# Kernel optimization log

Hardware: AMD Instinct MI355X
Metric: run time of the kernel (lower is better)

The kernel has to match this reference:

```python
import jax, jax.numpy as jnp
import numpy as np

B, S, D, H = 2, 2048, 1024, 16
HD = D // H  # 64
SCALE = HD ** -0.5


def setup_inputs() -> dict:
    key = jax.random.key(0)
    ks = jax.random.split(key, 11)
    std = D ** -0.5
    inp = {
        "q": jax.random.normal(ks[0], (B, S, D), jnp.float32),
        "k": jax.random.normal(ks[1], (B, S, D), jnp.float32),
        "v": jax.random.normal(ks[2], (B, S, D), jnp.float32),
        # causal mask: True = masked (strictly upper triangular)
        "attn_mask": jnp.triu(jnp.ones((S, S), jnp.bool_), k=1),
        "Wq": jax.random.normal(ks[3], (D, D), jnp.float32) * std,
        "bq": jnp.zeros((D,), jnp.float32),
        "Wk": jax.random.normal(ks[4], (D, D), jnp.float32) * std,
        "bk": jnp.zeros((D,), jnp.float32),
        "Wv": jax.random.normal(ks[5], (D, D), jnp.float32) * std,
        "bv": jnp.zeros((D,), jnp.float32),
        "Wo": jax.random.normal(ks[6], (D, D), jnp.float32) * std,
        "bo": jnp.zeros((D,), jnp.float32),
    }
    return inp


def reference(q, k, v, attn_mask, Wq, bq, Wk, bk, Wv, bv, Wo, bo):
    # projections (torch Linear: x @ W.T + b), split into heads: [B,H,S,HD]
    def heads(x, W, b):
        y = jnp.einsum("bsd,ed->bse", x, W) + b
        return y.reshape(B, S, H, HD).transpose(0, 2, 1, 3)

    qh = heads(q, Wq, bq)
    kh = heads(k, Wk, bk)
    vh = heads(v, Wv, bv)

    # scaled dot-product attention with mask (True = blocked)
    scores = jnp.einsum("bhqd,bhkd->bhqk", qh, kh) * SCALE
    scores = jnp.where(attn_mask[None, None, :, :], -jnp.inf, scores)
    weights = jax.nn.softmax(scores, axis=-1)
    out = jnp.einsum("bhqk,bhkd->bhqd", weights, vh)

    # merge heads and output projection
    out = out.transpose(0, 2, 1, 3).reshape(B, S, D)
    return jnp.einsum("bsd,ed->bse", out, Wo) + bo
```

## Files before the change

kernel.cpp:

```cpp
#include <hip/hip_runtime.h>
#include <hip/hip_bf16.h>

typedef __attribute__((ext_vector_type(8))) short bf16x8;
typedef __attribute__((ext_vector_type(4))) float f32x4;

#define NB 2
#define NS 2048
#define ND 1024
#define NH 16
#define NHD 64
#define ATTN_SCALE 0.125f

__device__ __forceinline__ unsigned short f2bf(float f) {
    union { float f; unsigned int u; } x; x.f = f;
    unsigned int r = x.u + 0x7fffu + ((x.u >> 16) & 1u);
    return (unsigned short)(r >> 16);
}

__device__ __forceinline__ void gload16(const void* g, void* l) {
    __builtin_amdgcn_global_load_lds(
        (const __attribute__((address_space(1))) unsigned int*)g,
        (__attribute__((address_space(3))) unsigned int*)l, 16, 0, 0);
}

__device__ __forceinline__ void cvt_store16(unsigned short* p,
        const float4& a0, const float4& a1, const float4& a2, const float4& a3) {
    uint4 u0, u1;
    u0.x = (unsigned)f2bf(a0.x) | ((unsigned)f2bf(a0.y) << 16);
    u0.y = (unsigned)f2bf(a0.z) | ((unsigned)f2bf(a0.w) << 16);
    u0.z = (unsigned)f2bf(a1.x) | ((unsigned)f2bf(a1.y) << 16);
    u0.w = (unsigned)f2bf(a1.z) | ((unsigned)f2bf(a1.w) << 16);
    u1.x = (unsigned)f2bf(a2.x) | ((unsigned)f2bf(a2.y) << 16);
    u1.y = (unsigned)f2bf(a2.z) | ((unsigned)f2bf(a2.w) << 16);
    u1.z = (unsigned)f2bf(a3.x) | ((unsigned)f2bf(a3.y) << 16);
    u1.w = (unsigned)f2bf(a3.z) | ((unsigned)f2bf(a3.w) << 16);
    ((uint4*)p)[0] = u0;
    ((uint4*)p)[1] = u1;
}

__global__ __launch_bounds__(256) void cvt_kernel(
    const float* __restrict__ s0, const float* __restrict__ s1,
    const float* __restrict__ s2, const float* __restrict__ s3,
    unsigned short* __restrict__ d0, unsigned short* __restrict__ d1,
    unsigned short* __restrict__ d2, unsigned short* __restrict__ d3, int n)
{
    const float* s = (blockIdx.y == 0) ? s0 : (blockIdx.y == 1) ? s1 : (blockIdx.y == 2) ? s2 : s3;
    unsigned short* d = (blockIdx.y == 0) ? d0 : (blockIdx.y == 1) ? d1 : (blockIdx.y == 2) ? d2 : d3;
    const int i = (blockIdx.x * 256 + threadIdx.x) * 8;
    if (i >= n) return;
    const float4* sp = (const float4*)(s + i);
    const float4 a = sp[0], b = sp[1];
    uint4 u;
    u.x = (unsigned)f2bf(a.x) | ((unsigned)f2bf(a.y) << 16);
    u.y = (unsigned)f2bf(a.z) | ((unsigned)f2bf(a.w) << 16);
    u.z = (unsigned)f2bf(b.x) | ((unsigned)f2bf(b.y) << 16);
    u.w = (unsigned)f2bf(b.z) | ((unsigned)f2bf(b.w) << 16);
    *(uint4*)(d + i) = u;
}

__global__ __launch_bounds__(256) void qkv2_kernel(
    const unsigned short* __restrict__ xq, const unsigned short* __restrict__ xk,
    const unsigned short* __restrict__ xv,
    const unsigned short* __restrict__ wq, const unsigned short* __restrict__ wk,
    const unsigned short* __restrict__ wv,
    const float* __restrict__ bq, const float* __restrict__ bk, const float* __restrict__ bv,
    unsigned short* __restrict__ qh, unsigned short* __restrict__ kh, unsigned short* __restrict__ vt)
{
    __shared__ __align__(16) unsigned short lds[2][2][128 * 32];
    const int t = threadIdx.x;
    const int lane = t & 63;
    const int wid = t >> 6;
    const int wm = wid >> 1, wn = wid & 1;
    const int lq = lane & 15, g = lane >> 4;
    const int bm = blockIdx.x;
    const int mat = blockIdx.y >> 3;
    const int bn = blockIdx.y & 7;

    const unsigned short* x = (mat == 0) ? xq : (mat == 1) ? xk : xv;
    const unsigned short* W = (mat == 0) ? wq : (mat == 1) ? wk : wv;
    const float* bias = (mat == 0) ? bq : (mat == 1) ? bk : bv;
    unsigned short* dst = (mat == 0) ? qh : (mat == 1) ? kh : vt;
    const float scale = (mat == 0) ? ATTN_SCALE : 1.0f;

    const char* abyte = (const char*)x;
    const char* bbyte = (const char*)W;
    const int rowl0 = (2 * wid + 0) * 16 + (lane >> 2);
    const int rowl1 = (2 * wid + 1) * 16 + (lane >> 2);
    const int colb = (lane & 3) * 16;
    const size_t abase0 = (size_t)(bm * 128 + rowl0) * 2048 + colb;
    const size_t abase1 = (size_t)(bm * 128 + rowl1) * 2048 + colb;
    const size_t bbase0 = (size_t)(bn * 128 + rowl0) * 2048 + colb;
    const size_t bbase1 = (size_t)(bn * 128 + rowl1) * 2048 + colb;

    f32x4 acc[4][4];
    const f32x4 zero = {0.f, 0.f, 0.f, 0.f};
#pragma unroll
    for (int m = 0; m < 4; ++m)
#pragma unroll
        for (int n = 0; n < 4; ++n) acc[m][n] = zero;

    auto STAGE = [&](int kt, int bufi) {
        const size_t ko = (size_t)kt * 64;
        gload16(abyte + abase0 + ko, (char*)&lds[bufi][0][0] + (2 * wid + 0) * 1024);
        gload16(abyte + abase1 + ko, (char*)&lds[bufi][0][0] + (2 * wid + 1) * 1024);
        gload16(bbyte + bbase0 + ko, (char*)&lds[bufi][1][0] + (2 * wid + 0) * 1024);
        gload16(bbyte + bbase1 + ko, (char*)&lds[bufi][1][0] + (2 * wid + 1) * 1024);
    };

    STAGE(0, 0);
    asm volatile("s_waitcnt vmcnt(0)" ::: "memory");
    __syncthreads();

    for (int kt = 0; kt < 32; ++kt) {
        const int cur = kt & 1;
        if (kt < 31) STAGE(kt + 1, cur ^ 1);
        bf16x8 af[4], bfr[4];
#pragma unroll
        for (int m = 0; m < 4; ++m)
            af[m] = *(const bf16x8*)&lds[cur][0][(wm * 64 + m * 16 + lq) * 32 + g * 8];
#pragma unroll
        for (int n = 0; n < 4; ++n)
            bfr[n] = *(const bf16x8*)&lds[cur][1][(wn * 64 + n * 16 + lq) * 32 + g * 8];
#pragma unroll
        for (int m = 0; m < 4; ++m)
#pragma unroll
            for (int n = 0; n < 4; ++n)
                acc[m][n] = __builtin_amdgcn_mfma_f32_16x16x32_bf16(af[m], bfr[n], acc[m][n], 0, 0, 0);
        __syncthreads();
    }

    const int row0 = bm * 128 + wm * 64;
    const int col0 = bn * 128 + wn * 64;
#pragma unroll
    for (int n = 0; n < 4; ++n) {
        const int col = col0 + n * 16 + lq;
        const float bb = bias[col];
        const int h = col >> 6, hd = col & 63;
#pragma unroll
        for (int m = 0; m < 4; ++m) {
#pragma unroll
            for (int r = 0; r < 4; ++r) {
                const int row = row0 + m * 16 + g * 4 + r;
                const int b = row >> 11, s = row & (NS - 1);
                const float v = (acc[m][n][r] + bb) * scale;
                size_t o;
                if (mat == 2) o = ((size_t)((b * NH + h) * NHD + hd)) * NS + s;
                else          o = ((size_t)((b * NH + h) * NS + s)) * NHD + hd;
                dst[o] = f2bf(v);
            }
        }
    }
}

__global__ __launch_bounds__(256, 3) void attn2_kernel(
    const unsigned short* __restrict__ qh, const unsigned short* __restrict__ kh,
    const unsigned short* __restrict__ vt, unsigned short* __restrict__ ao)
{
    __shared__ __align__(16) unsigned short klds[2][4096];
    __shared__ __align__(16) unsigned short vlds[2][4096];
    __shared__ __align__(16) unsigned short plds[4][32 * 72];
    const int t = threadIdx.x, lane = t & 63, wid = t >> 6;
    const int lq = lane & 15, g = lane >> 4;

    const int i = blockIdx.x;
    int bh, qblk;
    if (i < 256) { bh = i & 31; qblk = 15 - (i >> 5); }
    else { const int j = i - 256; bh = j & 31; qblk = j >> 5; }
    const int b = bh >> 4, h = bh & 15;

    const unsigned short* qb = qh + (size_t)bh * NS * NHD;
    const char* kbyte = (const char*)(kh + (size_t)bh * NS * NHD);
    const char* vbyte = (const char*)(vt + (size_t)bh * NS * NHD);
    unsigned short* pw = plds[wid];
    const int q0w = qblk * 128 + wid * 32;

    bf16x8 qf[2][2];
#pragma unroll
    for (int qs = 0; qs < 2; ++qs)
#pragma unroll
        for (int ks = 0; ks < 2; ++ks)
            qf[qs][ks] = *(const bf16x8*)&qb[(size_t)(q0w + qs * 16 + lq) * NHD + ks * 32 + g * 8];

    f32x4 accO[4][2];
    const f32x4 zero = {0.f, 0.f, 0.f, 0.f};
#pragma unroll
    for (int c = 0; c < 4; ++c) { accO[c][0] = zero; accO[c][1] = zero; }
    float mrun[2] = {-INFINITY, -INFINITY};
    float lsum[2] = {0.f, 0.f};

    const int off0 = (2 * wid + 0) * 1024 + lane * 16;
    const int off1 = (2 * wid + 1) * 1024 + lane * 16;
    const int swz0 = off0 ^ (((off0 >> 7) & 7) << 4);
    const int swz1 = off1 ^ (((off1 >> 7) & 7) << 4);
    const int vsrc0 = ((off0 >> 7) << 12) + (swz0 & 127);
    const int vsrc1 = ((off1 >> 7) << 12) + (swz1 & 127);

    auto STAGE = [&](int tile, int bufi) {
        const size_t kk = (size_t)tile * 8192;
        const size_t vv = (size_t)tile * 128;
        gload16(kbyte + kk + swz0, (char*)&klds[bufi][0] + (2 * wid + 0) * 1024);
        gload16(kbyte + kk + swz1, (char*)&klds[bufi][0] + (2 * wid + 1) * 1024);
        gload16(vbyte + vv + vsrc0, (char*)&vlds[bufi][0] + (2 * wid + 0) * 1024);
        gload16(vbyte + vv + vsrc1, (char*)&vlds[bufi][0] + (2 * wid + 1) * 1024);
    };

    const int T = 2 * qblk + 2;
    int buf = 0;
    STAGE(0, 0);
    asm volatile("s_waitcnt vmcnt(0)" ::: "memory");
    __syncthreads();

    for (int tile = 0; tile < T; ++tile) {
        const int kv0 = tile * 64;
        if (tile + 1 < T) STAGE(tile + 1, buf ^ 1);

        if (kv0 < q0w + 32) {
            f32x4 st[4][2];
#pragma unroll
            for (int kv = 0; kv < 4; ++kv) { st[kv][0] = zero; st[kv][1] = zero; }
#pragma unroll
            for (int ks = 0; ks < 2; ++ks) {
#pragma unroll
                for (int kv = 0; kv < 4; ++kv) {
                    const int lbyte = (kv * 16 + lq) * 128 + ks * 64 + g * 16;
                    const bf16x8 kf = *(const bf16x8*)((const char*)&klds[buf][0] + (lbyte ^ ((lq & 7) << 4)));
                    st[kv][0] = __builtin_amdgcn_mfma_f32_16x16x32_bf16(kf, qf[0][ks], st[kv][0], 0, 0, 0);
                    st[kv][1] = __builtin_amdgcn_mfma_f32_16x16x32_bf16(kf, qf[1][ks], st[kv][1], 0, 0, 0);
                }
            }
            if (kv0 + 63 > q0w) {
#pragma unroll
                for (int kv = 0; kv < 4; ++kv)
#pragma unroll
                    for (int r = 0; r < 4; ++r) {
                        const int kvi = kv0 + kv * 16 + g * 4 + r;
#pragma unroll
                        for (int qs = 0; qs < 2; ++qs) {
                            const int qi = q0w + qs * 16 + lq;
                            if (kvi > qi) st[kv][qs][r] = -1e30f;
                        }
                    }
            }
#pragma unroll
            for (int qs = 0; qs < 2; ++qs) {
                float tmax = st[0][qs][0];
#pragma unroll
                for (int kv = 0; kv < 4; ++kv)
#pragma unroll
                    for (int r = 0; r < 4; ++r) tmax = fmaxf(tmax, st[kv][qs][r]);
                tmax = fmaxf(tmax, __shfl_xor(tmax, 16));
                tmax = fmaxf(tmax, __shfl_xor(tmax, 32));
                const float mnew = fmaxf(mrun[qs], tmax);
                const float alpha = __expf(mrun[qs] - mnew);
                float ls = 0.f;
#pragma unroll
                for (int kv = 0; kv < 4; ++kv)
#pragma unroll
                    for (int r = 0; r < 4; ++r) {
                        const float p = __expf(st[kv][qs][r] - mnew);
                        st[kv][qs][r] = p;
                        ls += p;
                    }
                ls += __shfl_xor(ls, 16);
                ls += __shfl_xor(ls, 32);
                lsum[qs] = lsum[qs] * alpha + ls;
                mrun[qs] = mnew;
#pragma unroll
                for (int c = 0; c < 4; ++c) accO[c][qs] *= alpha;
#pragma unroll
                for (int kv = 0; kv < 4; ++kv) {
                    const unsigned u0 = (unsigned)f2bf(st[kv][qs][0]) | ((unsigned)f2bf(st[kv][qs][1]) << 16);
                    const unsigned u1 = (unsigned)f2bf(st[kv][qs][2]) | ((unsigned)f2bf(st[kv][qs][3]) << 16);
                    unsigned short* base = &pw[(qs * 16 + lq) * 72 + kv * 16 + g * 4];
                    *(unsigned*)base = u0;
                    *(unsigned*)(base + 2) = u1;
                }
            }
            asm volatile("s_waitcnt lgkmcnt(0)" ::: "memory");
#pragma unroll
            for (int ks = 0; ks < 2; ++ks) {
                const bf16x8 pb0 = *(const bf16x8*)&pw[(0 + lq) * 72 + ks * 32 + g * 8];
                const bf16x8 pb1 = *(const bf16x8*)&pw[(16 + lq) * 72 + ks * 32 + g * 8];
#pragma unroll
                for (int c = 0; c < 4; ++c) {
                    const int lbyte = (c * 16 + lq) * 128 + ks * 64 + g * 16;
                    const bf16x8 vf = *(const bf16x8*)((const char*)&vlds[buf][0] + (lbyte ^ ((lq & 7) << 4)));
                    accO[c][0] = __builtin_amdgcn_mfma_f32_16x16x32_bf16(vf, pb0, accO[c][0], 0, 0, 0);
                    accO[c][1] = __builtin_amdgcn_mfma_f32_16x16x32_bf16(vf, pb1, accO[c][1], 0, 0, 0);
                }
            }
        }
        __syncthreads();
        buf ^= 1;
    }

#pragma unroll
    for (int qs = 0; qs < 2; ++qs) {
        const float inv = 1.0f / lsum[qs];
        const int q = q0w + qs * 16 + lq;
        unsigned short* aobase = ao + ((size_t)b * NS + q) * ND + h * NHD;
#pragma unroll
        for (int c = 0; c < 4; ++c) {
            uint2 w2;
            w2.x = (unsigned)f2bf(accO[c][qs][0] * inv) | ((unsigned)f2bf(accO[c][qs][1] * inv) << 16);
            w2.y = (unsigned)f2bf(accO[c][qs][2] * inv) | ((unsigned)f2bf(accO[c][qs][3] * inv) << 16);
            *(uint2*)&aobase[c * 16 + g * 4] = w2;
        }
    }
}

__global__ __launch_bounds__(256) void oproj2_kernel(
    const unsigned short* __restrict__ ao, const unsigned short* __restrict__ wo,
    const float* __restrict__ bo, float* __restrict__ out)
{
    __shared__ __align__(16) unsigned short lds[2][2][128 * 32];
    const int t = threadIdx.x;
    const int lane = t & 63;
    const int wid = t >> 6;
    const int wm = wid >> 1, wn = wid & 1;
    const int lq = lane & 15, g = lane >> 4;
    const int bm = blockIdx.x;
    const int bn = blockIdx.y;

    const char* abyte = (const char*)ao;
    const char* bbyte = (const char*)wo;
    const int rowl0 = (2 * wid + 0) * 16 + (lane >> 2);
    const int rowl1 = (2 * wid + 1) * 16 + (lane >> 2);
    const int colb = (lane & 3) * 16;
    const size_t abase0 = (size_t)(bm * 128 + rowl0) * 2048 + colb;
    const size_t abase1 = (size_t)(bm * 128 + rowl1) * 2048 + colb;
    const size_t bbase0 = (size_t)(bn * 128 + rowl0) * 2048 + colb;
    const size_t bbase1 = (size_t)(bn * 128 + rowl1) * 2048 + colb;

    f32x4 acc[4][4];
    const f32x4 zero = {0.f, 0.f, 0.f, 0.f};
#pragma unroll
    for (int m = 0; m < 4; ++m)
#pragma unroll
        for (int n = 0; n < 4; ++n) acc[m][n] = zero;

    auto STAGE = [&](int kt, int bufi) {
        const size_t ko = (size_t)kt * 64;
        gload16(abyte + abase0 + ko, (char*)&lds[bufi][0][0] + (2 * wid + 0) * 1024);
        gload16(abyte + abase1 + ko, (char*)&lds[bufi][0][0] + (2 * wid + 1) * 1024);
        gload16(bbyte + bbase0 + ko, (char*)&lds[bufi][1][0] + (2 * wid + 0) * 1024);
        gload16(bbyte + bbase1 + ko, (char*)&lds[bufi][1][0] + (2 * wid + 1) * 1024);
    };

    STAGE(0, 0);
    asm volatile("s_waitcnt vmcnt(0)" ::: "memory");
    __syncthreads();

    for (int kt = 0; kt < 32; ++kt) {
        const int cur = kt & 1;
        if (kt < 31) STAGE(kt + 1, cur ^ 1);
        bf16x8 af[4], bfr[4];
#pragma unroll
        for (int m = 0; m < 4; ++m)
            af[m] = *(const bf16x8*)&lds[cur][0][(wm * 64 + m * 16 + lq) * 32 + g * 8];
#pragma unroll
        for (int n = 0; n < 4; ++n)
            bfr[n] = *(const bf16x8*)&lds[cur][1][(wn * 64 + n * 16 + lq) * 32 + g * 8];
#pragma unroll
        for (int m = 0; m < 4; ++m)
#pragma unroll
            for (int n = 0; n < 4; ++n)
                acc[m][n] = __builtin_amdgcn_mfma_f32_16x16x32_bf16(af[m], bfr[n], acc[m][n], 0, 0, 0);
        __syncthreads();
    }

    const int row0 = bm * 128 + wm * 64;
    const int col0 = bn * 128 + wn * 64;
#pragma unroll
    for (int n = 0; n < 4; ++n) {
        const int col = col0 + n * 16 + lq;
        const float bb = bo[col];
#pragma unroll
        for (int m = 0; m < 4; ++m) {
#pragma unroll
            for (int r = 0; r < 4; ++r) {
                const int row = row0 + m * 16 + g * 4 + r;
                out[(size_t)row * ND + col] = acc[m][n][r] + bb;
            }
        }
    }
}

__global__ __launch_bounds__(256) void qkv_proj_kernel(
    const float* __restrict__ xq, const float* __restrict__ xk, const float* __restrict__ xv,
    const float* __restrict__ Wq, const float* __restrict__ Wk, const float* __restrict__ Wv,
    const float* __restrict__ bq, const float* __restrict__ bk, const float* __restrict__ bv,
    unsigned short* __restrict__ qh, unsigned short* __restrict__ kh, unsigned short* __restrict__ vt)
{
    __shared__ __align__(16) unsigned short lds[2][2][128 * 32];
    const int t = threadIdx.x;
    const int lane = t & 63;
    const int wid = t >> 6;
    const int wm = wid >> 1, wn = wid & 1;
    const int lq = lane & 15, g = lane >> 4;
    const int bm = blockIdx.x;
    const int mat = blockIdx.y >> 3;
    const int bn = blockIdx.y & 7;

    const float* x = (mat == 0) ? xq : (mat == 1) ? xk : xv;
    const float* W = (mat == 0) ? Wq : (mat == 1) ? Wk : Wv;
    const float* bias = (mat == 0) ? bq : (mat == 1) ? bk : bv;
    unsigned short* dst = (mat == 0) ? qh : (mat == 1) ? kh : vt;
    const float scale = (mat == 0) ? ATTN_SCALE : 1.0f;

    const int srow = t >> 1;
    const int scol = (t & 1) << 4;
    const float* aptr = x + (size_t)(bm * 128 + srow) * ND + scol;
    const float* bptr = W + (size_t)(bn * 128 + srow) * ND + scol;
    const int soff = srow * 32 + scol;

    f32x4 acc[4][4];
    const f32x4 zero = {0.f, 0.f, 0.f, 0.f};
#pragma unroll
    for (int m = 0; m < 4; ++m)
#pragma unroll
        for (int n = 0; n < 4; ++n) acc[m][n] = zero;

    {
        const float4* ap = (const float4*)aptr;
        float4 A0 = ap[0], A1 = ap[1], A2 = ap[2], A3 = ap[3];
        const float4* bp = (const float4*)bptr;
        float4 B0 = bp[0], B1 = bp[1], B2 = bp[2], B3 = bp[3];
        cvt_store16(&lds[0][0][soff], A0, A1, A2, A3);
        cvt_store16(&lds[0][1][soff], B0, B1, B2, B3);
    }
    __syncthreads();

    for (int kt = 0; kt < ND / 32; ++kt) {
        const int cur = kt & 1;
        float4 A0, A1, A2, A3, B0, B1, B2, B3;
        if (kt < ND / 32 - 1) {
            const float4* ap = (const float4*)(aptr + (kt + 1) * 32);
            A0 = ap[0]; A1 = ap[1]; A2 = ap[2]; A3 = ap[3];
            const float4* bp = (const float4*)(bptr + (kt + 1) * 32);
            B0 = bp[0]; B1 = bp[1]; B2 = bp[2]; B3 = bp[3];
        }
        bf16x8 af[4], bfr[4];
#pragma unroll
        for (int m = 0; m < 4; ++m)
            af[m] = *(const bf16x8*)&lds[cur][0][(wm * 64 + m * 16 + lq) * 32 + g * 8];
#pragma unroll
        for (int n = 0; n < 4; ++n)
            bfr[n] = *(const bf16x8*)&lds[cur][1][(wn * 64 + n * 16 + lq) * 32 + g * 8];
#pragma unroll
        for (int m = 0; m < 4; ++m)
#pragma unroll
            for (int n = 0; n < 4; ++n)
                acc[m][n] = __builtin_amdgcn_mfma_f32_16x16x32_bf16(af[m], bfr[n], acc[m][n], 0, 0, 0);
        if (kt < ND / 32 - 1) {
            cvt_store16(&lds[cur ^ 1][0][soff], A0, A1, A2, A3);
            cvt_store16(&lds[cur ^ 1][1][soff], B0, B1, B2, B3);
        }
        __syncthreads();
    }

    const int row0 = bm * 128 + wm * 64;
    const int col0 = bn * 128 + wn * 64;
#pragma unroll
    for (int n = 0; n < 4; ++n) {
        const int col = col0 + n * 16 + lq;
        const float bb = bias[col];
        const int h = col >> 6, hd = col & 63;
#pragma unroll
        for (int m = 0; m < 4; ++m) {
#pragma unroll
            for (int r = 0; r < 4; ++r) {
                const int row = row0 + m * 16 + g * 4 + r;
                const int b = row >> 11, s = row & (NS - 1);
                const float v = (acc[m][n][r] + bb) * scale;
                size_t o;
                if (mat == 2) o = ((size_t)((b * NH + h) * NHD + hd)) * NS + s;
                else          o = ((size_t)((b * NH + h) * NS + s)) * NHD + hd;
                dst[o] = f2bf(v);
            }
        }
    }
}

__global__ __launch_bounds__(256) void out_proj_kernel(
    const unsigned short* __restrict__ ao, const float* __restrict__ Wo,
    const float* __restrict__ bo, float* __restrict__ out)
{
    __shared__ __align__(16) unsigned short lds[2][2][128 * 32];
    const int t = threadIdx.x;
    const int lane = t & 63;
    const int wid = t >> 6;
    const int wm = wid >> 1, wn = wid & 1;
    const int lq = lane & 15, g = lane >> 4;
    const int bm = blockIdx.x;
    const int bn = blockIdx.y;

    const int srow = t >> 1;
    const int scol = (t & 1) << 4;
    const unsigned short* aptr = ao + (size_t)(bm * 128 + srow) * ND + scol;
    const float* bptr = Wo + (size_t)(bn * 128 + srow) * ND + scol;
    const int soff = srow * 32 + scol;

    f32x4 acc[4][4];
    const f32x4 zero = {0.f, 0.f, 0.f, 0.f};
#pragma unroll
    for (int m = 0; m < 4; ++m)
#pragma unroll
        for (int n = 0; n < 4; ++n) acc[m][n] = zero;

    {
        const uint4* ap = (const uint4*)aptr;
        uint4 V0 = ap[0], V1 = ap[1];
        const float4* bp = (const float4*)bptr;
        float4 B0 = bp[0], B1 = bp[1], B2 = bp[2], B3 = bp[3];
        ((uint4*)&lds[0][0][soff])[0] = V0;
        ((uint4*)&lds[0][0][soff])[1] = V1;
        cvt_store16(&lds[0][1][soff], B0, B1, B2, B3);
    }
    __syncthreads();

    for (int kt = 0; kt < ND / 32; ++kt) {
        const int cur = kt & 1;
        uint4 V0, V1;
        float4 B0, B1, B2, B3;
        if (kt < ND / 32 - 1) {
            const uint4* ap = (const uint4*)(aptr + (kt + 1) * 32);
            V0 = ap[0]; V1 = ap[1];
            const float4* bp = (const float4*)(bptr + (kt + 1) * 32);
            B0 = bp[0]; B1 = bp[1]; B2 = bp[2]; B3 = bp[3];
        }
        bf16x8 af[4], bfr[4];
#pragma unroll
        for (int m = 0; m < 4; ++m)
            af[m] = *(const bf16x8*)&lds[cur][0][(wm * 64 + m * 16 + lq) * 32 + g * 8];
#pragma unroll
        for (int n = 0; n < 4; ++n)
            bfr[n] = *(const bf16x8*)&lds[cur][1][(wn * 64 + n * 16 + lq) * 32 + g * 8];
#pragma unroll
        for (int m = 0; m < 4; ++m)
#pragma unroll
            for (int n = 0; n < 4; ++n)
                acc[m][n] = __builtin_amdgcn_mfma_f32_16x16x32_bf16(af[m], bfr[n], acc[m][n], 0, 0, 0);
        if (kt < ND / 32 - 1) {
            ((uint4*)&lds[cur ^ 1][0][soff])[0] = V0;
            ((uint4*)&lds[cur ^ 1][0][soff])[1] = V1;
            cvt_store16(&lds[cur ^ 1][1][soff], B0, B1, B2, B3);
        }
        __syncthreads();
    }

    const int row0 = bm * 128 + wm * 64;
    const int col0 = bn * 128 + wn * 64;
#pragma unroll
    for (int n = 0; n < 4; ++n) {
        const int col = col0 + n * 16 + lq;
        const float bb = bo[col];
#pragma unroll
        for (int m = 0; m < 4; ++m) {
#pragma unroll
            for (int r = 0; r < 4; ++r) {
                const int row = row0 + m * 16 + g * 4 + r;
                out[(size_t)row * ND + col] = acc[m][n][r] + bb;
            }
        }
    }
}

extern "C" void kernel_launch(void* const* d_in, const int* in_sizes, int n_in,
                              void* d_out, int out_size, void* d_ws, size_t ws_size,
                              hipStream_t stream) {
    const float* q  = (const float*)d_in[0];
    const float* k  = (const float*)d_in[1];
    const float* v  = (const float*)d_in[2];
    const float* Wq = (const float*)d_in[4];
    const float* bq = (const float*)d_in[5];
    const float* Wk = (const float*)d_in[6];
    const float* bk = (const float*)d_in[7];
    const float* Wv = (const float*)d_in[8];
    const float* bv = (const float*)d_in[9];
    const float* Wo = (const float*)d_in[10];
    const float* bo = (const float*)d_in[11];

    const size_t elems = (size_t)NB * NS * ND;
    const size_t welems = (size_t)ND * ND;
    unsigned short* qh  = (unsigned short*)d_ws;
    unsigned short* kh  = qh + elems;
    unsigned short* vt  = kh + elems;
    unsigned short* ao  = vt + elems;
    unsigned short* xqb = ao + elems;
    unsigned short* xkb = xqb + elems;
    unsigned short* xvb = xkb + elems;
    unsigned short* wqb = xvb + elems;
    unsigned short* wkb = wqb + welems;
    unsigned short* wvb = wkb + welems;
    unsigned short* wob = wvb + welems;
    const size_t need = (size_t)(4 + 3) * elems * 2 + (size_t)4 * welems * 2;

    if (ws_size >= need) {
        cvt_kernel<<<dim3(2048, 3), 256, 0, stream>>>(q, k, v, q, xqb, xkb, xvb, xqb, (int)elems);
        cvt_kernel<<<dim3(512, 4), 256, 0, stream>>>(Wq, Wk, Wv, Wo, wqb, wkb, wvb, wob, (int)welems);
        qkv2_kernel<<<dim3(32, 24), 256, 0, stream>>>(xqb, xkb, xvb, wqb, wkb, wvb, bq, bk, bv, qh, kh, vt);
        attn2_kernel<<<dim3(512), 256, 0, stream>>>(qh, kh, vt, ao);
        oproj2_kernel<<<dim3(32, 8), 256, 0, stream>>>(ao, wob, bo, (float*)d_out);
    } else {
        qkv_proj_kernel<<<dim3(32, 24), 256, 0, stream>>>(q, k, v, Wq, Wk, Wv, bq, bk, bv, qh, kh, vt);
        attn2_kernel<<<dim3(512), 256, 0, stream>>>(qh, kh, vt, ao);
        out_proj_kernel<<<dim3(32, 8), 256, 0, stream>>>(ao, Wo, bo, (float*)d_out);
    }
}
```

Baseline: 254.4 us.

## Rewrite QKV projection GEMM with 256x256 tiles, 8 waves, swizzled LDS, ping-pong schedule

The QKV projection kernel moves from 128x128 tiles with K-step 32 on 4 waves to 256x256 tiles with K-step 64 on 8 waves. It uses XOR-swizzled LDS layouts to avoid bank conflicts and splits A and B prefetches across phases interleaved with MFMA blocks under priority and barrier control. The aim is more operand reuse per loaded byte and better overlap of global loads with compute. The cost is 192 blocks on a 256-CU device, which leaves CUs idle, plus higher register pressure from 32 accumulators per thread.

```diff
diff --git a/kernel.cpp b/kernel.cpp
--- a/kernel.cpp
+++ b/kernel.cpp
@@ -58,7 +58,7 @@
     *(uint4*)(d + i) = u;
 }
 
-__global__ __launch_bounds__(256) void qkv2_kernel(
+__global__ __launch_bounds__(512, 1) void qkv3_kernel(
     const unsigned short* __restrict__ xq, const unsigned short* __restrict__ xk,
     const unsigned short* __restrict__ xv,
     const unsigned short* __restrict__ wq, const unsigned short* __restrict__ wk,
@@ -66,15 +66,14 @@
     const float* __restrict__ bq, const float* __restrict__ bk, const float* __restrict__ bv,
     unsigned short* __restrict__ qh, unsigned short* __restrict__ kh, unsigned short* __restrict__ vt)
 {
-    __shared__ __align__(16) unsigned short lds[2][2][128 * 32];
+    __shared__ __align__(16) unsigned short ldsA[2][16384];
+    __shared__ __align__(16) unsigned short ldsB[2][16384];
     const int t = threadIdx.x;
-    const int lane = t & 63;
-    const int wid = t >> 6;
-    const int wm = wid >> 1, wn = wid & 1;
+    const int lane = t & 63, wid = t >> 6;
+    const int wr = wid >> 2, wc = wid & 3;
     const int lq = lane & 15, g = lane >> 4;
     const int bm = blockIdx.x;
-    const int mat = blockIdx.y >> 3;
-    const int bn = blockIdx.y & 7;
+    const int mat = blockIdx.y >> 2, bn = blockIdx.y & 3;
 
     const unsigned short* x = (mat == 0) ? xq : (mat == 1) ? xk : xv;
     const unsigned short* W = (mat == 0) ? wq : (mat == 1) ? wk : wv;
@@ -82,62 +81,131 @@
     unsigned short* dst = (mat == 0) ? qh : (mat == 1) ? kh : vt;
     const float scale = (mat == 0) ? ATTN_SCALE : 1.0f;
 
+    const int srccol = (((lane & 7) ^ (lane >> 3)) << 4);
+    const size_t abase = (size_t)(bm * 256 + wid * 8 + (lane >> 3)) * 2048 + srccol;
+    const size_t bbase = (size_t)(bn * 256 + wid * 8 + (lane >> 3)) * 2048 + srccol;
+    const int ldst = wid * 1024;
     const char* abyte = (const char*)x;
     const char* bbyte = (const char*)W;
-    const int rowl0 = (2 * wid + 0) * 16 + (lane >> 2);
-    const int rowl1 = (2 * wid + 1) * 16 + (lane >> 2);
-    const int colb = (lane & 3) * 16;
-    const size_t abase0 = (size_t)(bm * 128 + rowl0) * 2048 + colb;
-    const size_t abase1 = (size_t)(bm * 128 + rowl1) * 2048 + colb;
-    const size_t bbase0 = (size_t)(bn * 128 + rowl0) * 2048 + colb;
-    const size_t bbase1 = (size_t)(bn * 128 + rowl1) * 2048 + colb;
-
-    f32x4 acc[4][4];
+
+    f32x4 acc[8][4];
     const f32x4 zero = {0.f, 0.f, 0.f, 0.f};
 #pragma unroll
-    for (int m = 0; m < 4; ++m)
+    for (int m = 0; m < 8; ++m)
 #pragma unroll
         for (int n = 0; n < 4; ++n) acc[m][n] = zero;
 
-    auto STAGE = [&](int kt, int bufi) {
-        const size_t ko = (size_t)kt * 64;
-        gload16(abyte + abase0 + ko, (char*)&lds[bufi][0][0] + (2 * wid + 0) * 1024);
-        gload16(abyte + abase1 + ko, (char*)&lds[bufi][0][0] + (2 * wid + 1) * 1024);
-        gload16(bbyte + bbase0 + ko, (char*)&lds[bufi][1][0] + (2 * wid + 0) * 1024);
-        gload16(bbyte + bbase1 + ko, (char*)&lds[bufi][1][0] + (2 * wid + 1) * 1024);
+    auto STAGE_A = [&](int kt, int bufi) {
+        const size_t ko = (size_t)kt * 128;
+#pragma unroll
+        for (int p = 0; p < 4; ++p)
+            gload16(abyte + abase + (size_t)p * 131072 + ko,
+                    (char*)&ldsA[bufi][0] + p * 8192 + ldst);
     };
-
-    STAGE(0, 0);
+    auto STAGE_B = [&](int kt, int bufi) {
+        const size_t ko = (size_t)kt * 128;
+#pragma unroll
+        for (int p = 0; p < 4; ++p)
+            gload16(bbyte + bbase + (size_t)p * 131072 + ko,
+                    (char*)&ldsB[bufi][0] + p * 8192 + ldst);
+    };
+
+    const int swz = (lq & 7) << 4;
+    const int ac0 = (g * 16) ^ swz;
+    const int ac1 = (64 + g * 16) ^ swz;
+    const int arow = (wr * 128 + lq) * 128;
+    const int brow = (wc * 64 + lq) * 128;
+#define LDA(buf_, m_, ks_) (*(const bf16x8*)((const char*)&ldsA[buf_][0] + arow + (m_) * 2048 + ((ks_) ? ac1 : ac0)))
+#define LDB(buf_, n_, ks_) (*(const bf16x8*)((const char*)&ldsB[buf_][0] + brow + (n_) * 2048 + ((ks_) ? ac1 : ac0)))
+#define MFMA __builtin_amdgcn_mfma_f32_16x16x32_bf16
+
+    STAGE_A(0, 0);
+    STAGE_B(0, 0);
     asm volatile("s_waitcnt vmcnt(0)" ::: "memory");
     __syncthreads();
 
-    for (int kt = 0; kt < 32; ++kt) {
-        const int cur = kt & 1;
-        if (kt < 31) STAGE(kt + 1, cur ^ 1);
-        bf16x8 af[4], bfr[4];
-#pragma unroll
-        for (int m = 0; m < 4; ++m)
-            af[m] = *(const bf16x8*)&lds[cur][0][(wm * 64 + m * 16 + lq) * 32 + g * 8];
-#pragma unroll
-        for (int n = 0; n < 4; ++n)
-            bfr[n] = *(const bf16x8*)&lds[cur][1][(wn * 64 + n * 16 + lq) * 32 + g * 8];
-#pragma unroll
-        for (int m = 0; m < 4; ++m)
-#pragma unroll
-            for (int n = 0; n < 4; ++n)
-                acc[m][n] = __builtin_amdgcn_mfma_f32_16x16x32_bf16(af[m], bfr[n], acc[m][n], 0, 0, 0);
-        __syncthreads();
-    }
-
-    const int row0 = bm * 128 + wm * 64;
-    const int col0 = bn * 128 + wn * 64;
+    bf16x8 af[4][2], bfr[2][2], bf2[2][2];
+    int buf = 0;
+    for (int kt = 0; kt < 16; ++kt) {
+        const bool pre = (kt < 15);
+#pragma unroll
+        for (int m = 0; m < 4; ++m) { af[m][0] = LDA(buf, m, 0); af[m][1] = LDA(buf, m, 1); }
+#pragma unroll
+        for (int n = 0; n < 2; ++n) { bfr[n][0] = LDB(buf, n, 0); bfr[n][1] = LDB(buf, n, 1); }
+        if (pre) STAGE_A(kt + 1, buf ^ 1);
+        __builtin_amdgcn_s_barrier();
+        asm volatile("s_waitcnt lgkmcnt(0)" ::: "memory");
+        __builtin_amdgcn_sched_barrier(0);
+        __builtin_amdgcn_s_setprio(1);
+#pragma unroll
+        for (int m = 0; m < 4; ++m)
+#pragma unroll
+            for (int n = 0; n < 2; ++n) {
+                acc[m][n] = MFMA(af[m][0], bfr[n][0], acc[m][n], 0, 0, 0);
+                acc[m][n] = MFMA(af[m][1], bfr[n][1], acc[m][n], 0, 0, 0);
+            }
+        __builtin_amdgcn_s_setprio(0);
+        __builtin_amdgcn_s_barrier();
+
+#pragma unroll
+        for (int n = 0; n < 2; ++n) { bf2[n][0] = LDB(buf, n + 2, 0); bf2[n][1] = LDB(buf, n + 2, 1); }
+        if (pre) STAGE_B(kt + 1, buf ^ 1);
+        __builtin_amdgcn_s_barrier();
+        asm volatile("s_waitcnt lgkmcnt(0)" ::: "memory");
+        __builtin_amdgcn_sched_barrier(0);
+        __builtin_amdgcn_s_setprio(1);
+#pragma unroll
+        for (int m = 0; m < 4; ++m)
+#pragma unroll
+            for (int n = 0; n < 2; ++n) {
+                acc[m][n + 2] = MFMA(af[m][0], bf2[n][0], acc[m][n + 2], 0, 0, 0);
+                acc[m][n + 2] = MFMA(af[m][1], bf2[n][1], acc[m][n + 2], 0, 0, 0);
+            }
+        __builtin_amdgcn_s_setprio(0);
+        __builtin_amdgcn_s_barrier();
+
+#pragma unroll
+        for (int m = 0; m < 4; ++m) { af[m][0] = LDA(buf, m + 4, 0); af[m][1] = LDA(buf, m + 4, 1); }
+        __builtin_amdgcn_s_barrier();
+        asm volatile("s_waitcnt lgkmcnt(0)" ::: "memory");
+        __builtin_amdgcn_sched_barrier(0);
+        __builtin_amdgcn_s_setprio(1);
+#pragma unroll
+        for (int m = 0; m < 4; ++m)
+#pragma unroll
+            for (int n = 0; n < 2; ++n) {
+                acc[m + 4][n + 2] = MFMA(af[m][0], bf2[n][0], acc[m + 4][n + 2], 0, 0, 0);
+                acc[m + 4][n + 2] = MFMA(af[m][1], bf2[n][1], acc[m + 4][n + 2], 0, 0, 0);
+            }
+        __builtin_amdgcn_s_setprio(0);
+        __builtin_amdgcn_s_barrier();
+
+        __builtin_amdgcn_s_setprio(1);
+#pragma unroll
+        for (int m = 0; m < 4; ++m)
+#pragma unroll
+            for (int n = 0; n < 2; ++n) {
+                acc[m + 4][n] = MFMA(af[m][0], bfr[n][0], acc[m + 4][n], 0, 0, 0);
+                acc[m + 4][n] = MFMA(af[m][1], bfr[n][1], acc[m + 4][n], 0, 0, 0);
+            }
+        __builtin_amdgcn_s_setprio(0);
+        if (pre) asm volatile("s_waitcnt vmcnt(0)" ::: "memory");
+        __builtin_amdgcn_s_barrier();
+        buf ^= 1;
+    }
+#undef LDA
+#undef LDB
+#undef MFMA
+
+    const int row0 = bm * 256 + wr * 128;
+    const int col0 = bn * 256 + wc * 64;
 #pragma unroll
     for (int n = 0; n < 4; ++n) {
         const int col = col0 + n * 16 + lq;
         const float bb = bias[col];
         const int h = col >> 6, hd = col & 63;
 #pragma unroll
-        for (int m = 0; m < 4; ++m) {
+        for (int m = 0; m < 8; ++m) {
 #pragma unroll
             for (int r = 0; r < 4; ++r) {
                 const int row = row0 + m * 16 + g * 4 + r;
@@ -599,7 +667,7 @@
     if (ws_size >= need) {
         cvt_kernel<<<dim3(2048, 3), 256, 0, stream>>>(q, k, v, q, xqb, xkb, xvb, xqb, (int)elems);
         cvt_kernel<<<dim3(512, 4), 256, 0, stream>>>(Wq, Wk, Wv, Wo, wqb, wkb, wvb, wob, (int)welems);
-        qkv2_kernel<<<dim3(32, 24), 256, 0, stream>>>(xqb, xkb, xvb, wqb, wkb, wvb, bq, bk, bv, qh, kh, vt);
+        qkv3_kernel<<<dim3(16, 12), 512, 0, stream>>>(xqb, xkb, xvb, wqb, wkb, wvb, bq, bk, bv, qh, kh, vt);
         attn2_kernel<<<dim3(512), 256, 0, stream>>>(qh, kh, vt, ao);
         oproj2_kernel<<<dim3(32, 8), 256, 0, stream>>>(ao, wob, bo, (float*)d_out);
     } else {
```

Measured after the change: 270.8 us. 6.4% more time.

## Load K/V tiles directly from global into registers, drop shared staging

Applied to the files above, without the earlier changes.

The attention kernel no longer stages K and V tiles in shared memory with block-wide barriers. Each wave now loads its own K and V fragments straight from global memory into registers, with a software-pipelined ping-pong on K. Each wave also runs only as many tiles as its own causal extent needs, so the block-level __syncthreads goes away. In exchange every wave fetches the full K/V itself, a 4x redundancy that relies on L2/L1. Register pressure also rises, so launch bounds drop from 3 to 2 blocks per CU.

```diff
diff --git a/kernel.cpp b/kernel.cpp
--- a/kernel.cpp
+++ b/kernel.cpp
@@ -152,12 +152,10 @@
     }
 }
 
-__global__ __launch_bounds__(256, 3) void attn2_kernel(
+__global__ __launch_bounds__(256, 2) void attn3_kernel(
     const unsigned short* __restrict__ qh, const unsigned short* __restrict__ kh,
     const unsigned short* __restrict__ vt, unsigned short* __restrict__ ao)
 {
-    __shared__ __align__(16) unsigned short klds[2][4096];
-    __shared__ __align__(16) unsigned short vlds[2][4096];
     __shared__ __align__(16) unsigned short plds[4][32 * 72];
     const int t = threadIdx.x, lane = t & 63, wid = t >> 6;
     const int lq = lane & 15, g = lane >> 4;
@@ -169,8 +167,8 @@
     const int b = bh >> 4, h = bh & 15;
 
     const unsigned short* qb = qh + (size_t)bh * NS * NHD;
-    const char* kbyte = (const char*)(kh + (size_t)bh * NS * NHD);
-    const char* vbyte = (const char*)(vt + (size_t)bh * NS * NHD);
+    const unsigned short* kb = kh + (size_t)bh * NS * NHD;
+    const unsigned short* vb = vt + (size_t)bh * NS * NHD;
     unsigned short* pw = plds[wid];
     const int q0w = qblk * 128 + wid * 32;
 
@@ -188,110 +186,111 @@
     float mrun[2] = {-INFINITY, -INFINITY};
     float lsum[2] = {0.f, 0.f};
 
-    const int off0 = (2 * wid + 0) * 1024 + lane * 16;
-    const int off1 = (2 * wid + 1) * 1024 + lane * 16;
-    const int swz0 = off0 ^ (((off0 >> 7) & 7) << 4);
-    const int swz1 = off1 ^ (((off1 >> 7) & 7) << 4);
-    const int vsrc0 = ((off0 >> 7) << 12) + (swz0 & 127);
-    const int vsrc1 = ((off1 >> 7) << 12) + (swz1 & 127);
-
-    auto STAGE = [&](int tile, int bufi) {
-        const size_t kk = (size_t)tile * 8192;
-        const size_t vv = (size_t)tile * 128;
-        gload16(kbyte + kk + swz0, (char*)&klds[bufi][0] + (2 * wid + 0) * 1024);
-        gload16(kbyte + kk + swz1, (char*)&klds[bufi][0] + (2 * wid + 1) * 1024);
-        gload16(vbyte + vv + vsrc0, (char*)&vlds[bufi][0] + (2 * wid + 0) * 1024);
-        gload16(vbyte + vv + vsrc1, (char*)&vlds[bufi][0] + (2 * wid + 1) * 1024);
+    auto LOADK = [&](bf16x8 (&kf)[2][4], int tile) {
+        const int kv0 = tile * 64;
+#pragma unroll
+        for (int ks = 0; ks < 2; ++ks)
+#pragma unroll
+            for (int kv = 0; kv < 4; ++kv)
+                kf[ks][kv] = *(const bf16x8*)&kb[(size_t)(kv0 + kv * 16 + lq) * NHD + ks * 32 + g * 8];
     };
-
-    const int T = 2 * qblk + 2;
-    int buf = 0;
-    STAGE(0, 0);
-    asm volatile("s_waitcnt vmcnt(0)" ::: "memory");
-    __syncthreads();
-
-    for (int tile = 0; tile < T; ++tile) {
+    auto LOADV = [&](bf16x8 (&vf)[2][4], int tile) {
         const int kv0 = tile * 64;
-        if (tile + 1 < T) STAGE(tile + 1, buf ^ 1);
-
-        if (kv0 < q0w + 32) {
-            f32x4 st[4][2];
-#pragma unroll
-            for (int kv = 0; kv < 4; ++kv) { st[kv][0] = zero; st[kv][1] = zero; }
-#pragma unroll
-            for (int ks = 0; ks < 2; ++ks) {
-#pragma unroll
-                for (int kv = 0; kv < 4; ++kv) {
-                    const int lbyte = (kv * 16 + lq) * 128 + ks * 64 + g * 16;
-                    const bf16x8 kf = *(const bf16x8*)((const char*)&klds[buf][0] + (lbyte ^ ((lq & 7) << 4)));
-                    st[kv][0] = __builtin_amdgcn_mfma_f32_16x16x32_bf16(kf, qf[0][ks], st[kv][0], 0, 0, 0);
-                    st[kv][1] = __builtin_amdgcn_mfma_f32_16x16x32_bf16(kf, qf[1][ks], st[kv][1], 0, 0, 0);
+#pragma unroll
+        for (int ks = 0; ks < 2; ++ks)
+#pragma unroll
+            for (int c = 0; c < 4; ++c)
+                vf[ks][c] = *(const bf16x8*)&vb[(size_t)(c * 16 + lq) * NS + kv0 + ks * 32 + g * 8];
+    };
+
+    auto TILE = [&](int tile, bf16x8 (&kf)[2][4], bf16x8 (&vf)[2][4]) {
+        const int kv0 = tile * 64;
+        f32x4 st[4][2];
+#pragma unroll
+        for (int kv = 0; kv < 4; ++kv) { st[kv][0] = zero; st[kv][1] = zero; }
+#pragma unroll
+        for (int ks = 0; ks < 2; ++ks)
+#pragma unroll
+            for (int kv = 0; kv < 4; ++kv) {
+                st[kv][0] = __builtin_amdgcn_mfma_f32_16x16x32_bf16(kf[ks][kv], qf[0][ks], st[kv][0], 0, 0, 0);
+                st[kv][1] = __builtin_amdgcn_mfma_f32_16x16x32_bf16(kf[ks][kv], qf[1][ks], st[kv][1], 0, 0, 0);
+            }
+        if (kv0 + 63 > q0w) {
+#pragma unroll
+            for (int kv = 0; kv < 4; ++kv)
+#pragma unroll
+                for (int r = 0; r < 4; ++r) {
+                    const int kvi = kv0 + kv * 16 + g * 4 + r;
+#pragma unroll
+                    for (int qs = 0; qs < 2; ++qs) {
+                        const int qi = q0w + qs * 16 + lq;
+                        if (kvi > qi) st[kv][qs][r] = -1e30f;
+                    }
                 }
+        }
+#pragma unroll
+        for (int qs = 0; qs < 2; ++qs) {
+            float tmax = st[0][qs][0];
+#pragma unroll
+            for (int kv = 0; kv < 4; ++kv)
+#pragma unroll
+                for (int r = 0; r < 4; ++r) tmax = fmaxf(tmax, st[kv][qs][r]);
+            tmax = fmaxf(tmax, __shfl_xor(tmax, 16));
+            tmax = fmaxf(tmax, __shfl_xor(tmax, 32));
+            const float mnew = fmaxf(mrun[qs], tmax);
+            const float alpha = __expf(mrun[qs] - mnew);
+            float ls = 0.f;
+#pragma unroll
+            for (int kv = 0; kv < 4; ++kv)
+#pragma unroll
+                for (int r = 0; r < 4; ++r) {
+                    const float p = __expf(st[kv][qs][r] - mnew);
+                    st[kv][qs][r] = p;
+                    ls += p;
+                }
+            ls += __shfl_xor(ls, 16);
+            ls += __shfl_xor(ls, 32);
+            lsum[qs] = lsum[qs] * alpha + ls;
+            mrun[qs] = mnew;
+#pragma unroll
+            for (int c = 0; c < 4; ++c) accO[c][qs] *= alpha;
+#pragma unroll
+            for (int kv = 0; kv < 4; ++kv) {
+                const unsigned u0 = (unsigned)f2bf(st[kv][qs][0]) | ((unsigned)f2bf(st[kv][qs][1]) << 16);
+                const unsigned u1 = (unsigned)f2bf(st[kv][qs][2]) | ((unsigned)f2bf(st[kv][qs][3]) << 16);
+                unsigned short* base = &pw[(qs * 16 + lq) * 72 + kv * 16 + g * 4];
+                *(unsigned*)base = u0;
+                *(unsigned*)(base + 2) = u1;
             }
-            if (kv0 + 63 > q0w) {
-#pragma unroll
-                for (int kv = 0; kv < 4; ++kv)
-#pragma unroll
-                    for (int r = 0; r < 4; ++r) {
-                        const int kvi = kv0 + kv * 16 + g * 4 + r;
-#pragma unroll
-                        for (int qs = 0; qs < 2; ++qs) {
-                            const int qi = q0w + qs * 16 + lq;
-                            if (kvi > qi) st[kv][qs][r] = -1e30f;
-                        }
-                    }
+        }
+        asm volatile("s_waitcnt lgkmcnt(0)" ::: "memory");
+#pragma unroll
+        for (int ks = 0; ks < 2; ++ks) {
+            const bf16x8 pb0 = *(const bf16x8*)&pw[(0 + lq) * 72 + ks * 32 + g * 8];
+            const bf16x8 pb1 = *(const bf16x8*)&pw[(16 + lq) * 72 + ks * 32 + g * 8];
+#pragma unroll
+            for (int c = 0; c < 4; ++c) {
+                accO[c][0] = __builtin_amdgcn_mfma_f32_16x16x32_bf16(vf[ks][c], pb0, accO[c][0], 0, 0, 0);
+                accO[c][1] = __builtin_amdgcn_mfma_f32_16x16x32_bf16(vf[ks][c], pb1, accO[c][1], 0, 0, 0);
             }
-#pragma unroll
-            for (int qs = 0; qs < 2; ++qs) {
-                float tmax = st[0][qs][0];
-#pragma unroll
-                for (int kv = 0; kv < 4; ++kv)
-#pragma unroll
-                    for (int r = 0; r < 4; ++r) tmax = fmaxf(tmax, st[kv][qs][r]);
-                tmax = fmaxf(tmax, __shfl_xor(tmax, 16));
-                tmax = fmaxf(tmax, __shfl_xor(tmax, 32));
-                const float mnew = fmaxf(mrun[qs], tmax);
-                const float alpha = __expf(mrun[qs] - mnew);
-                float ls = 0.f;
-#pragma unroll
-                for (int kv = 0; kv < 4; ++kv)
-#pragma unroll
-                    for (int r = 0; r < 4; ++r) {
-                        const float p = __expf(st[kv][qs][r] - mnew);
-                        st[kv][qs][r] = p;
-                        ls += p;
-                    }
-                ls += __shfl_xor(ls, 16);
-                ls += __shfl_xor(ls, 32);
-                lsum[qs] = lsum[qs] * alpha + ls;
-                mrun[qs] = mnew;
-#pragma unroll
-                for (int c = 0; c < 4; ++c) accO[c][qs] *= alpha;
-#pragma unroll
-                for (int kv = 0; kv < 4; ++kv) {
-                    const unsigned u0 = (unsigned)f2bf(st[kv][qs][0]) | ((unsigned)f2bf(st[kv][qs][1]) << 16);
-                    const unsigned u1 = (unsigned)f2bf(st[kv][qs][2]) | ((unsigned)f2bf(st[kv][qs][3]) << 16);
-                    unsigned short* base = &pw[(qs * 16 + lq) * 72 + kv * 16 + g * 4];
-                    *(unsigned*)base = u0;
-                    *(unsigned*)(base + 2) = u1;
-                }
-            }
-            asm volatile("s_waitcnt lgkmcnt(0)" ::: "memory");
-#pragma unroll
-            for (int ks = 0; ks < 2; ++ks) {
-                const bf16x8 pb0 = *(const bf16x8*)&pw[(0 + lq) * 72 + ks * 32 + g * 8];
-                const bf16x8 pb1 = *(const bf16x8*)&pw[(16 + lq) * 72 + ks * 32 + g * 8];
-#pragma unroll
-                for (int c = 0; c < 4; ++c) {
-                    const int lbyte = (c * 16 + lq) * 128 + ks * 64 + g * 16;
-                    const bf16x8 vf = *(const bf16x8*)((const char*)&vlds[buf][0] + (lbyte ^ ((lq & 7) << 4)));
-                    accO[c][0] = __builtin_amdgcn_mfma_f32_16x16x32_bf16(vf, pb0, accO[c][0], 0, 0, 0);
-                    accO[c][1] = __builtin_amdgcn_mfma_f32_16x16x32_bf16(vf, pb1, accO[c][1], 0, 0, 0);
-                }
-            }
-        }
-        __syncthreads();
-        buf ^= 1;
+        }
+    };
+
+    const int Tw = ((q0w + 31) >> 6) + 1;
+    bf16x8 kfA[2][4], kfB[2][4], vf[2][4];
+    LOADK(kfA, 0);
+    int tt = 0;
+    for (; tt + 1 < Tw; tt += 2) {
+        LOADV(vf, tt);
+        LOADK(kfB, tt + 1);
+        TILE(tt, kfA, vf);
+        LOADV(vf, tt + 1);
+        if (tt + 2 < Tw) LOADK(kfA, tt + 2);
+        TILE(tt + 1, kfB, vf);
+    }
+    if (tt < Tw) {
+        LOADV(vf, tt);
+        TILE(tt, kfA, vf);
     }
 
 #pragma unroll
@@ -600,11 +599,11 @@
         cvt_kernel<<<dim3(2048, 3), 256, 0, stream>>>(q, k, v, q, xqb, xkb, xvb, xqb, (int)elems);
         cvt_kernel<<<dim3(512, 4), 256, 0, stream>>>(Wq, Wk, Wv, Wo, wqb, wkb, wvb, wob, (int)welems);
         qkv2_kernel<<<dim3(32, 24), 256, 0, stream>>>(xqb, xkb, xvb, wqb, wkb, wvb, bq, bk, bv, qh, kh, vt);
-        attn2_kernel<<<dim3(512), 256, 0, stream>>>(qh, kh, vt, ao);
+        attn3_kernel<<<dim3(512), 256, 0, stream>>>(qh, kh, vt, ao);
         oproj2_kernel<<<dim3(32, 8), 256, 0, stream>>>(ao, wob, bo, (float*)d_out);
     } else {
         qkv_proj_kernel<<<dim3(32, 24), 256, 0, stream>>>(q, k, v, Wq, Wk, Wv, bq, bk, bv, qh, kh, vt);
-        attn2_kernel<<<dim3(512), 256, 0, stream>>>(qh, kh, vt, ao);
+        attn3_kernel<<<dim3(512), 256, 0, stream>>>(qh, kh, vt, ao);
         out_proj_kernel<<<dim3(32, 8), 256, 0, stream>>>(ao, Wo, bo, (float*)d_out);
     }
 }
```

Result: no change. 258.5 us (+1.6%).
